# Kernel tuning notes

Measured on AMD Instinct MI355X. Metric: run time of the kernel, lower is better.

Reference implementation:

```python
import jax, jax.numpy as jnp
import numpy as np

VOCAB, EMBED, HIDDEN = 50257, 256, 512
BATCH, SEQ = 4, 2048


def posneg(x):
    # max(0,x) - |min(0,x)|  (mathematically the identity, computed as written)
    return jnp.maximum(jnp.zeros_like(x), x) - jnp.abs(jnp.minimum(jnp.zeros_like(x), x))


def setup_inputs() -> dict:
    key = jax.random.key(0)
    ks = jax.random.split(key, 10)
    s = 0.02
    return {
        "token_ids": jax.random.randint(ks[0], (BATCH, SEQ), 0, VOCAB),
        "emb_table": jax.random.normal(ks[1], (VOCAB, EMBED), jnp.float32) * s,
        "W1": jax.random.normal(ks[2], (EMBED, HIDDEN), jnp.float32) * s,
        "b1": jax.random.normal(ks[3], (HIDDEN,), jnp.float32) * s,
        "Wq": jax.random.normal(ks[4], (HIDDEN, HIDDEN), jnp.float32) * s,
        "bq": jax.random.normal(ks[5], (HIDDEN,), jnp.float32) * s,
        "Wk": jax.random.normal(ks[6], (HIDDEN, HIDDEN), jnp.float32) * s,
        "bk": jax.random.normal(ks[7], (HIDDEN,), jnp.float32) * s,
        "Wv": jax.random.normal(ks[8], (HIDDEN, HIDDEN), jnp.float32) * s,
        "bv": jax.random.normal(ks[9], (HIDDEN,), jnp.float32) * s,
    }


def reference(token_ids, emb_table, W1, b1, Wq, bq, Wk, bk, Wv, bv):
    emb = emb_table[token_ids]                      # [B,S,E]
    emb = posneg(emb)
    hidden = posneg(emb) @ W1 + b1                  # [B,S,H]
    hidden = posneg(hidden)
    act = jax.nn.gelu(hidden, approximate=False)
    act = posneg(act)
    q = posneg(act) @ Wq + bq
    k = posneg(act) @ Wk + bk
    v = posneg(act) @ Wv + bv
    q, k, v = posneg(q), posneg(k), posneg(v)
    # scaled_dot_product_attention (single head, hand-rolled)
    q, k = posneg(q), posneg(k)
    scores = jnp.einsum("bsh,bth->bst", q, k)       # [B,S,S]
    scores = posneg(scores) / jnp.sqrt(jnp.float32(q.shape[-1]))
    attn = jax.nn.softmax(scores, axis=-1)
    attn = posneg(attn)
    v = posneg(v)
    out = jnp.einsum("bst,bth->bsh", attn, v)       # [B,S,H]
    return posneg(out)
```

## Files before the change

kernel.cpp:

```cpp
#include <hip/hip_runtime.h>
#include <math.h>


typedef unsigned short u16;
typedef u16   u16x8 __attribute__((ext_vector_type(8)));
typedef short s16x8 __attribute__((ext_vector_type(8)));
typedef float f32x4 __attribute__((ext_vector_type(4)));
typedef float f32x8 __attribute__((ext_vector_type(8)));

static __device__ __forceinline__ u16 f2bf(float f) {
    unsigned u = __builtin_bit_cast(unsigned, f);
    u = (u + 0x7fffu + ((u >> 16) & 1u)) >> 16;
    return (u16)u;
}

static __device__ __forceinline__ void gload_lds16(const u16* g, u16* l) {
    __builtin_amdgcn_global_load_lds(
        (const __attribute__((address_space(1))) void*)g,
        (__attribute__((address_space(3))) void*)l, 16, 0, 0);
}

struct PArgs {
    const float* wsrc[4];
    u16*         wdst[4];
    int          wK[4];
    const float* emb;
    const int*   tok;
    u16*         embB;
};

__launch_bounds__(256)
__global__ void prep_k(PArgs p)
{
    const int z = blockIdx.z;
    if (z < 4) {
        const float* W = p.wsrc[z];
        u16* WT = p.wdst[z];
        const int K = p.wK[z];
        const int c0 = blockIdx.x * 64;
        const int r0 = blockIdx.y * 64;
        if (r0 >= K) return;
        __shared__ float T[64][65];
        const int t = threadIdx.x;
        const int col = t & 63;
        const int rb  = t >> 6;
#pragma unroll
        for (int i = 0; i < 16; ++i)
            T[i * 4 + rb][col] = W[(long)(r0 + i * 4 + rb) * 512 + c0 + col];
        __syncthreads();
#pragma unroll
        for (int i = 0; i < 16; ++i) {
            const int orow = i * 4 + rb;
            WT[(long)(c0 + orow) * K + r0 + col] = f2bf(T[col][orow]);
        }
    } else {
        const int b = (z - 4) * 64 + blockIdx.y * 8 + blockIdx.x;
        const int g = (b & 7) * 128 + (b >> 3);
        const int t = g * 2048 + threadIdx.x * 8;
        const int row = t >> 8;
        const int c8  = t & 255;
        f32x8 v = *(const f32x8*)(p.emb + (long)p.tok[row] * 256 + c8);
        u16x8 o;
#pragma unroll
        for (int j = 0; j < 8; ++j) o[j] = f2bf(v[j]);
        *(u16x8*)(p.embB + (long)row * 256 + c8) = o;
    }
}

struct GArgs {
    const u16* A; const u16* B; const float* bias; void* C;
    float* Cpart;
    float* lsum;
    u16 *qd, *kd, *vTd;
    const float *bq, *bk, *bv;
    int K, lda, ldb, ldc;
    long strA, strB, strC;
    float scale;
};

template <int TM, int NT, int KSUB, int OCC, int EPI, int CMODE, bool MX, bool SPLITK, bool XSW>
__launch_bounds__(256, OCC)
__global__ void gemm128(GArgs g)
{
    constexpr int BM  = TM * 32;
    constexpr int BN  = NT * 32;
    constexpr int ASZ = BM * 32;
    constexpr int BSZ = BN * 32;
    constexpr int BK  = 32 * KSUB;
    __shared__ u16 smem[2 * KSUB * (ASZ + BSZ)];
    __shared__ float invl[BM];
    u16* As = smem;
    u16* Bs = smem + 2 * KSUB * ASZ;

    const int bz    = blockIdx.z;
    const int batch = SPLITK ? (bz >> 1) : bz;
    const int kh    = SPLITK ? (bz & 1) : 0;
    const u16* A = g.A + g.strA * batch + (SPLITK ? kh * 1024 : 0);
    const u16* B = g.B + g.strB * batch + (SPLITK ? kh * 1024 : 0);

    int m0, n0;
    if (XSW) {
        const int lid = blockIdx.y * gridDim.x + blockIdx.x;
        const int xcd = lid & 7;
        const int j   = lid >> 3;
        const int mper = gridDim.y >> 3;
        m0 = (xcd * mper + (j % mper)) * BM;
        n0 = (j / mper) * BN;
    } else {
        m0 = (MX ? blockIdx.x : blockIdx.y) * BM;
        n0 = (MX ? blockIdx.y : blockIdx.x) * BN;
    }

    const int t = threadIdx.x;
    const int w = t >> 6;
    const int lane = t & 63;
    const int quad = lane >> 4;
    const int l16  = lane & 15;
    const int wm = w >> 1, wn = w & 1;

    if (CMODE == 4 && t < BM) {
        float l = 0.0f;
#pragma unroll
        for (int j = 0; j < 16; ++j)
            l += g.lsum[(long)j * 8192 + batch * 2048 + m0 + t];
        invl[t] = 1.0f / l;
    }

    const int srow = w * 16 + (lane >> 2);
    const int skc  = (((lane & 3) ^ ((lane >> 2) & 3)) * 8);
    const u16* ga = A + (long)(m0 + srow) * g.lda + skc;
    const u16* gb = B + (long)(n0 + srow) * g.ldb + skc;
    const long a64 = (long)64 * g.lda;
    const long b64 = (long)64 * g.ldb;

    auto stage = [&](int buf, int k0) {
#pragma unroll
        for (int s = 0; s < KSUB; ++s) {
            u16* la = As + (buf * KSUB + s) * ASZ + w * 512;
            u16* lb = Bs + (buf * KSUB + s) * BSZ + w * 512;
#pragma unroll
            for (int i = 0; i < TM / 2; ++i)
                gload_lds16(ga + i * a64 + k0 + s * 32, la + i * 2048);
#pragma unroll
            for (int i = 0; i < NT / 2; ++i)
                gload_lds16(gb + i * b64 + k0 + s * 32, lb + i * 2048);
        }
    };

    f32x4 acc[TM][NT] = {};
    const int K = SPLITK ? 1024 : g.K;
    const int qsw = quad ^ (l16 & 3);

    stage(0, 0);
    int cur = 0;
    for (int k0 = 0; k0 < K; k0 += BK) {
        __syncthreads();
        if (k0 + BK < K) stage(cur ^ 1, k0 + BK);

#pragma unroll
        for (int s = 0; s < KSUB; ++s) {
            const u16* as = As + (cur * KSUB + s) * ASZ;
            const u16* bs = Bs + (cur * KSUB + s) * BSZ;
            s16x8 af[TM], bf[NT];
#pragma unroll
            for (int x = 0; x < TM; ++x)
                af[x] = *(const s16x8*)&as[(wm * (TM * 16) + x * 16 + l16) * 32 + qsw * 8];
#pragma unroll
            for (int y = 0; y < NT; ++y)
                bf[y] = *(const s16x8*)&bs[(wn * (NT * 16) + y * 16 + l16) * 32 + qsw * 8];
#pragma unroll
            for (int x = 0; x < TM; ++x)
#pragma unroll
                for (int y = 0; y < NT; ++y)
                    acc[x][y] = __builtin_amdgcn_mfma_f32_16x16x32_bf16(af[x], bf[y], acc[x][y], 0, 0, 0);
        }
        cur ^= 1;
    }

    if (CMODE == 2 && n0 >= 1024) {
        u16* T = smem;
        __syncthreads();
#pragma unroll
        for (int y = 0; y < NT; ++y) {
            const int crel = wn * (NT * 16) + y * 16 + l16;
            const float bval = g.bv[n0 - 1024 + crel];
#pragma unroll
            for (int x = 0; x < TM; ++x)
#pragma unroll
                for (int r = 0; r < 4; ++r) {
                    const int rrel = wm * (TM * 16) + x * 16 + quad * 4 + r;
                    T[crel * 72 + rrel] = f2bf(acc[x][y][r] + bval);
                }
        }
        __syncthreads();
        const int vb  = m0 >> 11;
        const int pos = m0 & 2047;
        u16* dst = g.vTd + (long)vb * (512l * 2048) + (long)(n0 - 1024) * 2048 + pos;
#pragma unroll
        for (int i = 0; i < BN / 32; ++i) {
            const int c  = i * 32 + (t >> 3);
            const int ms = (t & 7) * 8;
            *(u16x8*)(dst + (long)c * 2048 + ms) = *(const u16x8*)&T[c * 72 + ms];
        }
        return;
    }

    float rs[TM][4];
    if (CMODE == 3)
#pragma unroll
        for (int x = 0; x < TM; ++x)
#pragma unroll
            for (int r = 0; r < 4; ++r) rs[x][r] = 0.0f;

#pragma unroll
    for (int y = 0; y < NT; ++y) {
        const int col = n0 + wn * (NT * 16) + y * 16 + l16;
        float bval = 0.0f;
        if (CMODE == 2)
            bval = col < 512 ? g.bq[col] : g.bk[col - 512];
        else if (EPI >= 1)
            bval = g.bias[col];
#pragma unroll
        for (int x = 0; x < TM; ++x) {
#pragma unroll
            for (int r = 0; r < 4; ++r) {
                const int row = m0 + wm * (TM * 16) + x * 16 + quad * 4 + r;
                float v = acc[x][y][r] * g.scale + bval;
                if (EPI == 2) v = 0.5f * v * (1.0f + erff(v * 0.70710678118654752f));
                if (CMODE == 3) {
                    const float e = __expf(v);
                    rs[x][r] += e;
                    ((u16*)g.C + g.strC * batch)[(long)row * g.ldc + col] = f2bf(e);
                } else if (CMODE == 2) {
                    u16* dst = col < 512 ? g.qd : g.kd;
                    dst[(long)row * 512 + (col & 511)] = f2bf(v);
                } else if (CMODE == 4) {
                    ((float*)g.C + g.strC * batch)[(long)row * g.ldc + col] = v * invl[row - m0];
                } else if (SPLITK) {
                    float* dst = kh ? g.Cpart : (float*)g.C;
                    dst[g.strC * batch + (long)row * g.ldc + col] = v;
                } else if (CMODE == 1) {
                    ((float*)g.C + g.strC * batch)[(long)row * g.ldc + col] = v;
                } else {
                    ((u16*)g.C + g.strC * batch)[(long)row * g.ldc + col] = f2bf(v);
                }
            }
        }
    }

    if (CMODE == 3) {
#pragma unroll
        for (int x = 0; x < TM; ++x) {
#pragma unroll
            for (int r = 0; r < 4; ++r) {
                float s = rs[x][r];
                s += __shfl_xor(s, 1, 64);
                s += __shfl_xor(s, 2, 64);
                s += __shfl_xor(s, 4, 64);
                s += __shfl_xor(s, 8, 64);
                if (l16 == 0) {
                    const int row = m0 + wm * (TM * 16) + x * 16 + quad * 4 + r;
                    g.lsum[(long)(2 * blockIdx.x + wn) * 8192 + batch * 2048 + row] = s;
                }
            }
        }
    }
}

extern "C" void kernel_launch(void* const* d_in, const int* in_sizes, int n_in,
                              void* d_out, int out_size, void* d_ws, size_t ws_size,
                              hipStream_t stream)
{
    const int*   tok = (const int*)d_in[0];
    const float* emb = (const float*)d_in[1];
    const float* W1  = (const float*)d_in[2];
    const float* b1  = (const float*)d_in[3];
    const float* Wq  = (const float*)d_in[4];
    const float* bq  = (const float*)d_in[5];
    const float* Wk  = (const float*)d_in[6];
    const float* bk  = (const float*)d_in[7];
    const float* Wv  = (const float*)d_in[8];
    const float* bv  = (const float*)d_in[9];
    float* out = (float*)d_out;

    u16* act   = (u16*)d_out;
    u16* wbase = act + 8192l * 512;
    u16* W1T = wbase;
    u16* WqT = wbase + 131072;
    u16* WkT = WqT + 262144;
    u16* WvT = WkT + 262144;

    char* ws = (char*)d_ws;
    u16* q     = (u16*)(ws);
    u16* k     = (u16*)(ws + (8l  << 20));
    u16* vT    = (u16*)(ws + (16l << 20));
    u16* sc    = (u16*)(ws + (24l << 20));
    float* lsum = (float*)(ws + (56l << 20));
    u16* embB  = sc;

    const dim3 blk(256);
    const float iscl = 0.044194173824159216f;
    const long  TB = 2048l * 512;
    const long  SS = 2048l * 2048;

    PArgs p;
    p.wsrc[0] = W1; p.wsrc[1] = Wq; p.wsrc[2] = Wk; p.wsrc[3] = Wv;
    p.wdst[0] = W1T; p.wdst[1] = WqT; p.wdst[2] = WkT; p.wdst[3] = WvT;
    p.wK[0] = 256; p.wK[1] = 512; p.wK[2] = 512; p.wK[3] = 512;
    p.emb = emb; p.tok = tok; p.embB = embB;
    prep_k<<<dim3(8, 8, 20), blk, 0, stream>>>(p);

    {
        GArgs a = {};
        a.A = embB; a.B = W1T; a.bias = b1; a.C = act;
        a.K = 256; a.lda = 256; a.ldb = 256; a.ldc = 512; a.scale = 1.0f;
        gemm128<2, 4, 2, 2, 2, 0, false, false, true><<<dim3(4, 128, 1), blk, 0, stream>>>(a);
    }
    {
        GArgs a = {};
        a.A = act; a.B = WqT; a.K = 512; a.lda = 512; a.ldb = 512; a.scale = 1.0f;
        a.qd = q; a.kd = k; a.vTd = vT; a.bq = bq; a.bk = bk; a.bv = bv;
        gemm128<2, 8, 1, 2, 0, 2, false, false, true><<<dim3(6, 128, 1), blk, 0, stream>>>(a);
    }
    {
        GArgs a = {};
        a.A = q; a.B = k; a.C = sc; a.lsum = lsum;
        a.K = 512; a.lda = 512; a.ldb = 512; a.ldc = 2048;
        a.strA = TB; a.strB = TB; a.strC = SS; a.scale = iscl;
        gemm128<4, 8, 1, 2, 0, 3, false, false, false><<<dim3(8, 16, 4), blk, 0, stream>>>(a);
    }
    {
        GArgs a = {};
        a.A = sc; a.B = vT; a.C = out; a.lsum = lsum;
        a.K = 2048; a.lda = 2048; a.ldb = 2048; a.ldc = 512;
        a.strA = SS; a.strB = TB; a.strC = TB; a.scale = 1.0f;
        gemm128<2, 4, 2, 2, 0, 4, true, false, false><<<dim3(32, 4, 4), blk, 0, stream>>>(a);
    }
}
```

Before: 194.2 us.

## Add triple-buffered LDS pipeline with partial vmcnt waits to GEMM kernels

Adds a PIPE template option that uses three LDS buffers and keeps two stages of global-to-LDS loads in flight. Each iteration waits only until the older stage has landed, using a hardcoded s_waitcnt vmcnt(6), instead of a full __syncthreads. This is meant to hide global load latency better in three of the four GEMMs, though not the QKV projection. It costs more shared memory, which can lower occupancy, and the hardcoded wait count is only correct while the loads per stage equal six.

```diff
diff --git a/kernel.cpp b/kernel.cpp
--- a/kernel.cpp
+++ b/kernel.cpp
@@ -78,7 +78,8 @@
     float scale;
 };
 
-template <int TM, int NT, int KSUB, int OCC, int EPI, int CMODE, bool MX, bool SPLITK, bool XSW>
+template <int TM, int NT, int KSUB, int OCC, int PIPE, int EPI, int CMODE,
+          bool MX, bool SPLITK, bool XSW>
 __launch_bounds__(256, OCC)
 __global__ void gemm128(GArgs g)
 {
@@ -87,10 +88,13 @@
     constexpr int ASZ = BM * 32;
     constexpr int BSZ = BN * 32;
     constexpr int BK  = 32 * KSUB;
-    __shared__ u16 smem[2 * KSUB * (ASZ + BSZ)];
+    constexpr int NBUF = (PIPE == 1) ? 3 : 2;
+    static_assert(PIPE == 0 || (TM / 2 + NT / 2) * KSUB == 6,
+                  "PIPE=1 hardcodes s_waitcnt vmcnt(6) == loads per stage");
+    __shared__ u16 smem[NBUF * KSUB * (ASZ + BSZ)];
     __shared__ float invl[BM];
     u16* As = smem;
-    u16* Bs = smem + 2 * KSUB * ASZ;
+    u16* Bs = smem + NBUF * KSUB * ASZ;
 
     const int bz    = blockIdx.z;
     const int batch = SPLITK ? (bz >> 1) : bz;
@@ -151,16 +155,11 @@
     const int K = SPLITK ? 1024 : g.K;
     const int qsw = quad ^ (l16 & 3);
 
-    stage(0, 0);
-    int cur = 0;
-    for (int k0 = 0; k0 < K; k0 += BK) {
-        __syncthreads();
-        if (k0 + BK < K) stage(cur ^ 1, k0 + BK);
-
+    auto compute = [&](int buf) {
 #pragma unroll
         for (int s = 0; s < KSUB; ++s) {
-            const u16* as = As + (cur * KSUB + s) * ASZ;
-            const u16* bs = Bs + (cur * KSUB + s) * BSZ;
+            const u16* as = As + (buf * KSUB + s) * ASZ;
+            const u16* bs = Bs + (buf * KSUB + s) * BSZ;
             s16x8 af[TM], bf[NT];
 #pragma unroll
             for (int x = 0; x < TM; ++x)
@@ -174,7 +173,29 @@
                 for (int y = 0; y < NT; ++y)
                     acc[x][y] = __builtin_amdgcn_mfma_f32_16x16x32_bf16(af[x], bf[y], acc[x][y], 0, 0, 0);
         }
-        cur ^= 1;
+    };
+
+    if constexpr (PIPE == 1) {
+        const int nt = K / BK;
+        stage(0, 0);
+        if (nt > 1) stage(1, BK);
+        for (int tt = 0; tt < nt; ++tt) {
+            if (tt + 1 < nt) asm volatile("s_waitcnt vmcnt(6)" ::: "memory");
+            else             asm volatile("s_waitcnt vmcnt(0)" ::: "memory");
+            __builtin_amdgcn_s_barrier();
+            __builtin_amdgcn_sched_barrier(0);
+            if (tt + 2 < nt) stage((tt + 2) % 3, (tt + 2) * BK);
+            compute(tt % 3);
+        }
+    } else {
+        stage(0, 0);
+        int cur = 0;
+        for (int k0 = 0; k0 < K; k0 += BK) {
+            __syncthreads();
+            if (k0 + BK < K) stage(cur ^ 1, k0 + BK);
+            compute(cur);
+            cur ^= 1;
+        }
     }
 
     if (CMODE == 2 && n0 >= 1024) {
@@ -314,26 +335,26 @@
         GArgs a = {};
         a.A = embB; a.B = W1T; a.bias = b1; a.C = act;
         a.K = 256; a.lda = 256; a.ldb = 256; a.ldc = 512; a.scale = 1.0f;
-        gemm128<2, 4, 2, 2, 2, 0, false, false, true><<<dim3(4, 128, 1), blk, 0, stream>>>(a);
+        gemm128<2, 4, 2, 2, 1, 2, 0, false, false, true><<<dim3(4, 128, 1), blk, 0, stream>>>(a);
     }
     {
         GArgs a = {};
         a.A = act; a.B = WqT; a.K = 512; a.lda = 512; a.ldb = 512; a.scale = 1.0f;
         a.qd = q; a.kd = k; a.vTd = vT; a.bq = bq; a.bk = bk; a.bv = bv;
-        gemm128<2, 8, 1, 2, 0, 2, false, false, true><<<dim3(6, 128, 1), blk, 0, stream>>>(a);
+        gemm128<2, 8, 1, 2, 0, 0, 2, false, false, true><<<dim3(6, 128, 1), blk, 0, stream>>>(a);
     }
     {
         GArgs a = {};
         a.A = q; a.B = k; a.C = sc; a.lsum = lsum;
         a.K = 512; a.lda = 512; a.ldb = 512; a.ldc = 2048;
         a.strA = TB; a.strB = TB; a.strC = SS; a.scale = iscl;
-        gemm128<4, 8, 1, 2, 0, 3, false, false, false><<<dim3(8, 16, 4), blk, 0, stream>>>(a);
+        gemm128<4, 8, 1, 2, 1, 0, 3, false, false, false><<<dim3(8, 16, 4), blk, 0, stream>>>(a);
     }
     {
         GArgs a = {};
         a.A = sc; a.B = vT; a.C = out; a.lsum = lsum;
         a.K = 2048; a.lda = 2048; a.ldb = 2048; a.ldc = 512;
         a.strA = SS; a.strB = TB; a.strC = TB; a.scale = 1.0f;
-        gemm128<2, 4, 2, 2, 0, 4, true, false, false><<<dim3(32, 4, 4), blk, 0, stream>>>(a);
-    }
-}
+        gemm128<2, 4, 2, 2, 1, 0, 4, true, false, false><<<dim3(32, 4, 4), blk, 0, stream>>>(a);
+    }
+}
```

After: 194.8 us. About the same (+0.3%).
